# Optimization experiments

Hardware: AMD Instinct MI355X
Metric: run time of the kernel (lower is better)

Reference implementation:

```python
import jax, jax.numpy as jnp
import numpy as np
from jax import lax

BN_EPS = 1e-5


def _spatial_gate(x, w, g, b, m, v):
    # x: [N, C, H, W]; ChannelPool -> [N, 2, H, W]; 7x7 conv -> [N,1,H,W]; BN (eval); sigmoid gate
    comp = jnp.stack([jnp.max(x, axis=1), jnp.mean(x, axis=1)], axis=1)
    o = lax.conv_general_dilated(comp, w, (1, 1), [(3, 3), (3, 3)],
                                 dimension_numbers=('NCHW', 'OIHW', 'NCHW'))
    o = (o - m[None, :, None, None]) * lax.rsqrt(v + BN_EPS)[None, :, None, None] \
        * g[None, :, None, None] + b[None, :, None, None]
    s = jax.nn.sigmoid(o)
    return x * s


def _eca_sort(x, w_eca):
    # global avg pool -> sort channels desc -> 1D conv over sorted seq -> sigmoid -> unsort -> gate
    y = jnp.mean(x, axis=(2, 3))               # [N, C]
    order = jnp.argsort(-y, axis=1)            # descending sort indices
    rank = jnp.argsort(order, axis=1)          # inverse permutation
    ys = jnp.take_along_axis(y, order, axis=1)  # sorted descending
    k = w_eca.shape[-1]
    p = k // 2
    o = lax.conv_general_dilated(ys[:, None, :], w_eca, (1,), [(p, p)],
                                 dimension_numbers=('NCH', 'OIH', 'NCH'))[:, 0, :]
    sig = jax.nn.sigmoid(o)
    yr = jnp.take_along_axis(sig, rank, axis=1)  # reorder back per original index_select(rank)
    return x * yr[:, :, None, None]


def setup_inputs() -> dict:
    key = jax.random.key(0)
    ks = jax.random.split(key, 6)
    N, C, H, W = 32, 256, 56, 56
    inp = {
        'x': jax.random.normal(ks[0], (N, C, H, W), dtype=jnp.float32),
        'weight': jax.random.normal(ks[1], (1,), dtype=jnp.float32),
        'w_h': jax.random.normal(ks[2], (1, 2, 7, 7), dtype=jnp.float32) * 0.1,
        'g_h': jnp.ones((1,), jnp.float32), 'b_h': jnp.zeros((1,), jnp.float32),
        'm_h': jnp.zeros((1,), jnp.float32), 'v_h': jnp.ones((1,), jnp.float32),
        'w_w': jax.random.normal(ks[3], (1, 2, 7, 7), dtype=jnp.float32) * 0.1,
        'g_w': jnp.ones((1,), jnp.float32), 'b_w': jnp.zeros((1,), jnp.float32),
        'm_w': jnp.zeros((1,), jnp.float32), 'v_w': jnp.ones((1,), jnp.float32),
        'w_s': jax.random.normal(ks[4], (1, 2, 7, 7), dtype=jnp.float32) * 0.1,
        'g_s': jnp.ones((1,), jnp.float32), 'b_s': jnp.zeros((1,), jnp.float32),
        'm_s': jnp.zeros((1,), jnp.float32), 'v_s': jnp.ones((1,), jnp.float32),
        'w_eca': jax.random.normal(ks[5], (1, 1, 5), dtype=jnp.float32) * 0.3,
    }
    return inp


def reference(x, weight, w_h, g_h, b_h, m_h, v_h, w_w, g_w, b_w, m_w, v_w,
              w_s, g_s, b_s, m_s, v_s, w_eca):
    # branch 1: gate over H-as-channel (permute 0,2,1,3)
    xh = jnp.transpose(x, (0, 2, 1, 3))
    x11 = jnp.transpose(_spatial_gate(xh, w_h, g_h, b_h, m_h, v_h), (0, 2, 1, 3))
    # branch 2: gate over W-as-channel (permute 0,3,2,1)
    xw = jnp.transpose(x, (0, 3, 2, 1))
    x21 = jnp.transpose(_spatial_gate(xw, w_w, g_w, b_w, m_w, v_w), (0, 3, 2, 1))
    # branch 3: eca with sort/unsort
    x31 = _eca_sort(x, w_eca)
    # branch 4: plain spatial gate
    xo = _spatial_gate(x, w_s, g_s, b_s, m_s, v_s)
    return 0.23779 * xo + 0.24695 * x11 + 0.24365 * x21 + 0.27173 * x31
```

## Files before the change

### kernel.cpp

```cpp
#include <hip/hip_runtime.h>
#include <math.h>

#define N_ 32
#define C_ 256
#define H_ 56
#define W_ 56
#define HW_ (H_*W_)
#define HW4_ (HW_/4)
#define CHW_ (C_*HW_)
#define NHW_ (N_*HW_)
#define NHW4_ (NHW_/4)
#define NCW_ (N_*C_*W_)
#define NHC_ (N_*H_*C_)
#define BN_EPS_ 1e-5f

#define TLD 60
#define PLANES_PER_BLK 8
#define NB_PL 1024

#define SM_BUF1 3360
#define SM_CPMX 6720
#define SM_CPSM (6720 + 224)
#define SM_TOT  (6720 + 448)

#define F4MAX(a,b) do { (a).x=fmaxf((a).x,(b).x); (a).y=fmaxf((a).y,(b).y); \
                        (a).z=fmaxf((a).z,(b).z); (a).w=fmaxf((a).w,(b).w); } while(0)
#define F4ADD(a,b) do { (a).x+=(b).x; (a).y+=(b).y; (a).z+=(b).z; (a).w+=(b).w; } while(0)

__global__ __launch_bounds__(256) void pools_k(
        const float* __restrict__ x,
        float* __restrict__ maxH, float* __restrict__ meanH,
        float* __restrict__ maxW, float* __restrict__ meanW,
        float* __restrict__ pmx, float* __restrict__ psm,
        float* __restrict__ y) {
    __shared__ float smem[SM_TOT];
    int b = blockIdx.x;
    int tid = threadIdx.x;
    const float4* x4 = (const float4*)x;
    float* buf0 = smem;
    float* buf1 = smem + SM_BUF1;
    float* cpmx = smem + SM_CPMX;
    float* cpsm = smem + SM_CPSM;
    int pb0 = b * PLANES_PER_BLK;
    float4 r0, r1, r2, r3;
    int row0 = tid / 14,          col0 = (tid % 14) * 4;
    int row1 = (tid + 256) / 14,  col1 = ((tid + 256) % 14) * 4;
    int row2 = (tid + 512) / 14,  col2 = ((tid + 512) % 14) * 4;
    int row3 = (tid + 768) / 14,  col3 = ((tid + 768) % 14) * 4;
    float4 amx0, amx1, amx2, amx3, asm0, asm1, asm2, asm3;
    amx0 = amx1 = amx2 = amx3 = make_float4(-INFINITY, -INFINITY, -INFINITY, -INFINITY);
    asm0 = asm1 = asm2 = asm3 = make_float4(0.f, 0.f, 0.f, 0.f);
    {
        size_t base = (size_t)pb0 * HW4_;
        r0 = x4[base + tid];
        r1 = x4[base + 256 + tid];
        r2 = x4[base + 512 + tid];
        if (tid < 16) r3 = x4[base + 768 + tid];
        F4MAX(amx0, r0); F4ADD(asm0, r0);
        F4MAX(amx1, r1); F4ADD(asm1, r1);
        F4MAX(amx2, r2); F4ADD(asm2, r2);
        if (tid < 16) { F4MAX(amx3, r3); F4ADD(asm3, r3); }
        *(float4*)&buf0[row0 * TLD + col0] = r0;
        *(float4*)&buf0[row1 * TLD + col1] = r1;
        *(float4*)&buf0[row2 * TLD + col2] = r2;
        if (tid < 16) *(float4*)&buf0[row3 * TLD + col3] = r3;
    }
    __syncthreads();
    for (int k = 0; k < PLANES_PER_BLK; ++k) {
        float* cur = (k & 1) ? buf1 : buf0;
        float* nxt = (k & 1) ? buf0 : buf1;
        int pb = pb0 + k;
        int n = pb >> 8, c = pb & 255;
        if (k < PLANES_PER_BLK - 1) {
            size_t base = (size_t)(pb + 1) * HW4_;
            r0 = x4[base + tid];
            r1 = x4[base + 256 + tid];
            r2 = x4[base + 512 + tid];
            if (tid < 16) r3 = x4[base + 768 + tid];
        }
        if (tid < 224) {
            int w = tid % 56, hq = tid / 56;
            const float* base = &cur[(hq * 14) * TLD + w];
            float mx = -INFINITY, sm = 0.f;
            #pragma unroll
            for (int hh = 0; hh < 14; ++hh) {
                float v = base[hh * TLD];
                mx = fmaxf(mx, v); sm += v;
            }
            cpmx[hq * 56 + w] = mx;
            cpsm[hq * 56 + w] = sm;
        }
        __syncthreads();
        float colsum = 0.f;
        if (tid < 56) {
            float mx = cpmx[tid], sm = cpsm[tid];
            #pragma unroll
            for (int j = 1; j < 4; ++j) {
                mx = fmaxf(mx, cpmx[j * 56 + tid]);
                sm += cpsm[j * 56 + tid];
            }
            int o = (n * C_ + c) * W_ + tid;
            maxH[o] = mx;
            meanH[o] = sm * (1.f / H_);
            colsum = sm;
        }
        if (tid < 64) {
            float t = colsum;
            #pragma unroll
            for (int off = 32; off >= 1; off >>= 1) t += __shfl_xor(t, off);
            if (tid == 0) y[n * C_ + c] = t * (1.f / HW_);
        }
        if (tid < 224) {
            int h = tid >> 2, kq = tid & 3;
            const float* base = &cur[h * TLD + kq * 14];
            float mx = -INFINITY, sm = 0.f;
            #pragma unroll
            for (int kk = 0; kk < 14; ++kk) {
                float v = base[kk];
                mx = fmaxf(mx, v); sm += v;
            }
            mx = fmaxf(mx, __shfl_xor(mx, 1)); sm += __shfl_xor(sm, 1);
            mx = fmaxf(mx, __shfl_xor(mx, 2)); sm += __shfl_xor(sm, 2);
            if (kq == 0) {
                int o = (n * H_ + h) * C_ + c;
                maxW[o] = mx;
                meanW[o] = sm * (1.f / W_);
            }
        }
        if (k < PLANES_PER_BLK - 1) {
            F4MAX(amx0, r0); F4ADD(asm0, r0);
            F4MAX(amx1, r1); F4ADD(asm1, r1);
            F4MAX(amx2, r2); F4ADD(asm2, r2);
            if (tid < 16) { F4MAX(amx3, r3); F4ADD(asm3, r3); }
            *(float4*)&nxt[row0 * TLD + col0] = r0;
            *(float4*)&nxt[row1 * TLD + col1] = r1;
            *(float4*)&nxt[row2 * TLD + col2] = r2;
            if (tid < 16) *(float4*)&nxt[row3 * TLD + col3] = r3;
        }
        __syncthreads();
    }
    {
        float4* PM = (float4*)pmx + (size_t)b * HW4_;
        float4* PS = (float4*)psm + (size_t)b * HW4_;
        PM[tid] = amx0;        PS[tid] = asm0;
        PM[tid + 256] = amx1;  PS[tid + 256] = asm1;
        PM[tid + 512] = amx2;  PS[tid + 512] = asm2;
        if (tid < 16) { PM[tid + 768] = amx3; PS[tid + 768] = asm3; }
    }
}

__global__ __launch_bounds__(256) void cpool_final_k(
        const float* __restrict__ pmx, const float* __restrict__ psm,
        float* __restrict__ maxC, float* __restrict__ meanC) {
    int t = blockIdx.x * 256 + threadIdx.x;
    int n = t / HW4_, hw4 = t - n * HW4_;
    const float4* PM = (const float4*)pmx + (size_t)(n * 32) * HW4_ + hw4;
    const float4* PS = (const float4*)psm + (size_t)(n * 32) * HW4_ + hw4;
    float4 mx = make_float4(-INFINITY, -INFINITY, -INFINITY, -INFINITY);
    float4 sm = make_float4(0.f, 0.f, 0.f, 0.f);
    #pragma unroll 8
    for (int g = 0; g < 32; ++g) {
        float4 v = PM[(size_t)g * HW4_];
        float4 s = PS[(size_t)g * HW4_];
        F4MAX(mx, v);
        F4ADD(sm, s);
    }
    sm.x *= (1.f / C_); sm.y *= (1.f / C_); sm.z *= (1.f / C_); sm.w *= (1.f / C_);
    ((float4*)maxC)[t] = mx;
    ((float4*)meanC)[t] = sm;
}

template <int R, int Cc>
__device__ __forceinline__ void conv7_part(int t, const float* __restrict__ p0,
                                           const float* __restrict__ p1,
                                           const float* __restrict__ wt,
                                           float g, float bb, float m, float v,
                                           float* __restrict__ out) {
    const int per = R * Cc;
    int n = t / per;
    int r2 = t - n * per;
    int i = r2 / Cc, j = r2 - i * Cc;
    const float* b0 = p0 + (size_t)n * per;
    const float* b1 = p1 + (size_t)n * per;
    float acc = 0.f;
    #pragma unroll
    for (int ki = 0; ki < 7; ++ki) {
        int ii = i + ki - 3;
        if (ii < 0 || ii >= R) continue;
        #pragma unroll
        for (int kj = 0; kj < 7; ++kj) {
            int jj = j + kj - 3;
            if (jj < 0 || jj >= Cc) continue;
            int idx = ii * Cc + jj;
            acc += b0[idx] * wt[ki * 7 + kj] + b1[idx] * wt[49 + ki * 7 + kj];
        }
    }
    float o = (acc - m) * rsqrtf(v + BN_EPS_) * g + bb;
    out[t] = 1.f / (1.f + expf(-o));
}

#define NB_SS (NHW_ / 256)
#define NB_SH (NCW_ / 256)
#define NB_SW (NHC_ / 256)

__global__ __launch_bounds__(256) void conv_eca_k(
        const float* __restrict__ maxC, const float* __restrict__ meanC,
        const float* __restrict__ maxH, const float* __restrict__ meanH,
        const float* __restrict__ maxW, const float* __restrict__ meanW,
        const float* __restrict__ w_s, const float* __restrict__ g_s,
        const float* __restrict__ b_s, const float* __restrict__ m_s,
        const float* __restrict__ v_s,
        const float* __restrict__ w_h, const float* __restrict__ g_h,
        const float* __restrict__ b_h, const float* __restrict__ m_h,
        const float* __restrict__ v_h,
        const float* __restrict__ w_w, const float* __restrict__ g_w,
        const float* __restrict__ b_w, const float* __restrict__ m_w,
        const float* __restrict__ v_w,
        const float* __restrict__ y, const float* __restrict__ w_eca,
        float* __restrict__ s_s, float* __restrict__ s_h, float* __restrict__ s_w,
        float* __restrict__ gate) {
    __shared__ float sv[C_];
    __shared__ int si[C_];
    int b = blockIdx.x;
    int tid = threadIdx.x;
    if (b < NB_SS) {
        conv7_part<H_, W_>(b * 256 + tid, maxC, meanC, w_s, g_s[0], b_s[0], m_s[0],
                           v_s[0], s_s);
    } else if (b < NB_SS + NB_SH) {
        conv7_part<C_, W_>((b - NB_SS) * 256 + tid, maxH, meanH, w_h, g_h[0], b_h[0],
                           m_h[0], v_h[0], s_h);
    } else if (b < NB_SS + NB_SH + NB_SW) {
        conv7_part<H_, C_>((b - NB_SS - NB_SH) * 256 + tid, maxW, meanW, w_w, g_w[0],
                           b_w[0], m_w[0], v_w[0], s_w);
    } else {
        int n = b - (NB_SS + NB_SH + NB_SW);
        sv[tid] = y[n * C_ + tid];
        si[tid] = tid;
        __syncthreads();
        for (int k = 2; k <= C_; k <<= 1) {
            for (int j = k >> 1; j > 0; j >>= 1) {
                int ixj = tid ^ j;
                if (ixj > tid) {
                    float v1 = sv[tid], v2 = sv[ixj];
                    int i1 = si[tid], i2 = si[ixj];
                    bool before = (v1 > v2) || (v1 == v2 && i1 < i2);
                    bool dir = ((tid & k) == 0);
                    if (dir ? !before : before) {
                        sv[tid] = v2; sv[ixj] = v1;
                        si[tid] = i2; si[ixj] = i1;
                    }
                }
                __syncthreads();
            }
        }
        float o = 0.f;
        #pragma unroll
        for (int j = 0; j < 5; ++j) {
            int p = tid + j - 2;
            if (p >= 0 && p < C_) o += sv[p] * w_eca[j];
        }
        gate[n * C_ + si[tid]] = 1.f / (1.f + expf(-o));
    }
}

__global__ __launch_bounds__(256) void apply_k(
        const float* __restrict__ x, const float* __restrict__ s_s,
        const float* __restrict__ s_h, const float* __restrict__ s_w,
        const float* __restrict__ gate, float* __restrict__ out) {
    int t0 = blockIdx.x * 512 + threadIdx.x;
    #pragma unroll
    for (int r = 0; r < 2; ++r) {
        int t = t0 + r * 256;
        int f = t * 4;
        int n = f / CHW_;
        int rem = f - n * CHW_;
        int c = rem / HW_;
        int hw = rem - c * HW_;
        int h = hw / W_;
        int w = hw - h * W_;
        float4 xv = ((const float4*)x)[t];
        float4 s4 = *(const float4*)(s_s + (size_t)n * HW_ + hw);
        float4 h4 = *(const float4*)(s_h + ((size_t)n * C_ + c) * W_ + w);
        float sw = s_w[((size_t)n * H_ + h) * C_ + c];
        float ge = gate[n * C_ + c];
        float base = 0.24365f * sw + 0.27173f * ge;
        float4 o;
        o.x = xv.x * (0.23779f * s4.x + 0.24695f * h4.x + base);
        o.y = xv.y * (0.23779f * s4.y + 0.24695f * h4.y + base);
        o.z = xv.z * (0.23779f * s4.z + 0.24695f * h4.z + base);
        o.w = xv.w * (0.23779f * s4.w + 0.24695f * h4.w + base);
        ((float4*)out)[t] = o;
    }
}

extern "C" void kernel_launch(void* const* d_in, const int* in_sizes, int n_in,
                              void* d_out, int out_size, void* d_ws, size_t ws_size,
                              hipStream_t stream) {
    const float* x     = (const float*)d_in[0];
    const float* w_h   = (const float*)d_in[2];
    const float* g_h   = (const float*)d_in[3];
    const float* b_h   = (const float*)d_in[4];
    const float* m_h   = (const float*)d_in[5];
    const float* v_h   = (const float*)d_in[6];
    const float* w_w   = (const float*)d_in[7];
    const float* g_w   = (const float*)d_in[8];
    const float* b_w   = (const float*)d_in[9];
    const float* m_w   = (const float*)d_in[10];
    const float* v_w   = (const float*)d_in[11];
    const float* w_s   = (const float*)d_in[12];
    const float* g_s   = (const float*)d_in[13];
    const float* b_s   = (const float*)d_in[14];
    const float* m_s   = (const float*)d_in[15];
    const float* v_s   = (const float*)d_in[16];
    const float* w_eca = (const float*)d_in[17];
    float* out = (float*)d_out;

    float* ws    = (float*)d_ws;
    float* maxC  = ws;
    float* meanC = maxC  + NHW_;
    float* maxH  = meanC + NHW_;
    float* meanH = maxH  + NCW_;
    float* maxW  = meanH + NCW_;
    float* meanW = maxW  + NHC_;
    float* s_s   = meanW + NHC_;
    float* s_h   = s_s   + NHW_;
    float* s_w   = s_h   + NCW_;
    float* yv    = s_w   + NHC_;
    float* gate  = yv    + N_ * C_;
    float* pmx   = gate  + N_ * C_;
    float* psm   = pmx   + NB_PL * HW_;

    pools_k<<<NB_PL, 256, 0, stream>>>(x, maxH, meanH, maxW, meanW, pmx, psm, yv);

    cpool_final_k<<<NHW4_ / 256, 256, 0, stream>>>(pmx, psm, maxC, meanC);

    int conv_blocks = NB_SS + NB_SH + NB_SW + N_;
    conv_eca_k<<<conv_blocks, 256, 0, stream>>>(maxC, meanC, maxH, meanH, maxW, meanW,
                                                w_s, g_s, b_s, m_s, v_s,
                                                w_h, g_h, b_h, m_h, v_h,
                                                w_w, g_w, b_w, m_w, v_w,
                                                yv, w_eca, s_s, s_h, s_w, gate);

    apply_k<<<(N_ * CHW_ / 4) / 512, 256, 0, stream>>>(x, s_s, s_h, s_w, gate, out);
}
```

Measured before the change: 104.8 us.

## Store W-branch pooled maps channel-major and transpose conv weights accordingly

The W-branch pooled max/mean and its gate are now stored as [N,C,H] instead of [N,H,C]. The conv uses transposed weight indexing so the result is unchanged. The aim is coalesced stores in pools_k, where consecutive h map to contiguous addresses, and more local gate reads in apply_k. The W-pool computation is also moved before the barrier, and launch bounds with a minimum of 4 blocks are added to the two pooling kernels, which may constrain register allocation.

```diff
diff --git a/kernel.cpp b/kernel.cpp
--- a/kernel.cpp
+++ b/kernel.cpp
@@ -27,10 +27,10 @@
                         (a).z=fmaxf((a).z,(b).z); (a).w=fmaxf((a).w,(b).w); } while(0)
 #define F4ADD(a,b) do { (a).x+=(b).x; (a).y+=(b).y; (a).z+=(b).z; (a).w+=(b).w; } while(0)
 
-__global__ __launch_bounds__(256) void pools_k(
+__global__ __launch_bounds__(256, 4) void pools_k(
         const float* __restrict__ x,
         float* __restrict__ maxH, float* __restrict__ meanH,
-        float* __restrict__ maxW, float* __restrict__ meanW,
+        float* __restrict__ maxWt, float* __restrict__ meanWt,
         float* __restrict__ pmx, float* __restrict__ psm,
         float* __restrict__ y) {
     __shared__ float smem[SM_TOT];
@@ -90,6 +90,23 @@
             cpmx[hq * 56 + w] = mx;
             cpsm[hq * 56 + w] = sm;
         }
+        if (tid < 224) {
+            int h = tid >> 2, kq = tid & 3;
+            const float* base = &cur[h * TLD + kq * 14];
+            float mx = -INFINITY, sm = 0.f;
+            #pragma unroll
+            for (int kk = 0; kk < 14; ++kk) {
+                float v = base[kk];
+                mx = fmaxf(mx, v); sm += v;
+            }
+            mx = fmaxf(mx, __shfl_xor(mx, 1)); sm += __shfl_xor(sm, 1);
+            mx = fmaxf(mx, __shfl_xor(mx, 2)); sm += __shfl_xor(sm, 2);
+            if (kq == 0) {
+                int o = (n * C_ + c) * H_ + h;
+                maxWt[o] = mx;
+                meanWt[o] = sm * (1.f / W_);
+            }
+        }
         __syncthreads();
         float colsum = 0.f;
         if (tid < 56) {
@@ -109,23 +126,6 @@
             #pragma unroll
             for (int off = 32; off >= 1; off >>= 1) t += __shfl_xor(t, off);
             if (tid == 0) y[n * C_ + c] = t * (1.f / HW_);
-        }
-        if (tid < 224) {
-            int h = tid >> 2, kq = tid & 3;
-            const float* base = &cur[h * TLD + kq * 14];
-            float mx = -INFINITY, sm = 0.f;
-            #pragma unroll
-            for (int kk = 0; kk < 14; ++kk) {
-                float v = base[kk];
-                mx = fmaxf(mx, v); sm += v;
-            }
-            mx = fmaxf(mx, __shfl_xor(mx, 1)); sm += __shfl_xor(sm, 1);
-            mx = fmaxf(mx, __shfl_xor(mx, 2)); sm += __shfl_xor(sm, 2);
-            if (kq == 0) {
-                int o = (n * H_ + h) * C_ + c;
-                maxW[o] = mx;
-                meanW[o] = sm * (1.f / W_);
-            }
         }
         if (k < PLANES_PER_BLK - 1) {
             F4MAX(amx0, r0); F4ADD(asm0, r0);
@@ -149,7 +149,7 @@
     }
 }
 
-__global__ __launch_bounds__(256) void cpool_final_k(
+__global__ __launch_bounds__(256, 4) void cpool_final_k(
         const float* __restrict__ pmx, const float* __restrict__ psm,
         float* __restrict__ maxC, float* __restrict__ meanC) {
     int t = blockIdx.x * 256 + threadIdx.x;
@@ -170,7 +170,7 @@
     ((float4*)meanC)[t] = sm;
 }
 
-template <int R, int Cc>
+template <int R, int Cc, bool TR>
 __device__ __forceinline__ void conv7_part(int t, const float* __restrict__ p0,
                                            const float* __restrict__ p1,
                                            const float* __restrict__ wt,
@@ -192,7 +192,8 @@
             int jj = j + kj - 3;
             if (jj < 0 || jj >= Cc) continue;
             int idx = ii * Cc + jj;
-            acc += b0[idx] * wt[ki * 7 + kj] + b1[idx] * wt[49 + ki * 7 + kj];
+            int wi = TR ? (kj * 7 + ki) : (ki * 7 + kj);
+            acc += b0[idx] * wt[wi] + b1[idx] * wt[49 + wi];
         }
     }
     float o = (acc - m) * rsqrtf(v + BN_EPS_) * g + bb;
@@ -206,7 +207,7 @@
 __global__ __launch_bounds__(256) void conv_eca_k(
         const float* __restrict__ maxC, const float* __restrict__ meanC,
         const float* __restrict__ maxH, const float* __restrict__ meanH,
-        const float* __restrict__ maxW, const float* __restrict__ meanW,
+        const float* __restrict__ maxWt, const float* __restrict__ meanWt,
         const float* __restrict__ w_s, const float* __restrict__ g_s,
         const float* __restrict__ b_s, const float* __restrict__ m_s,
         const float* __restrict__ v_s,
@@ -217,21 +218,21 @@
         const float* __restrict__ b_w, const float* __restrict__ m_w,
         const float* __restrict__ v_w,
         const float* __restrict__ y, const float* __restrict__ w_eca,
-        float* __restrict__ s_s, float* __restrict__ s_h, float* __restrict__ s_w,
+        float* __restrict__ s_s, float* __restrict__ s_h, float* __restrict__ s_wt,
         float* __restrict__ gate) {
     __shared__ float sv[C_];
     __shared__ int si[C_];
     int b = blockIdx.x;
     int tid = threadIdx.x;
     if (b < NB_SS) {
-        conv7_part<H_, W_>(b * 256 + tid, maxC, meanC, w_s, g_s[0], b_s[0], m_s[0],
-                           v_s[0], s_s);
+        conv7_part<H_, W_, false>(b * 256 + tid, maxC, meanC, w_s, g_s[0], b_s[0],
+                                  m_s[0], v_s[0], s_s);
     } else if (b < NB_SS + NB_SH) {
-        conv7_part<C_, W_>((b - NB_SS) * 256 + tid, maxH, meanH, w_h, g_h[0], b_h[0],
-                           m_h[0], v_h[0], s_h);
+        conv7_part<C_, W_, false>((b - NB_SS) * 256 + tid, maxH, meanH, w_h, g_h[0],
+                                  b_h[0], m_h[0], v_h[0], s_h);
     } else if (b < NB_SS + NB_SH + NB_SW) {
-        conv7_part<H_, C_>((b - NB_SS - NB_SH) * 256 + tid, maxW, meanW, w_w, g_w[0],
-                           b_w[0], m_w[0], v_w[0], s_w);
+        conv7_part<C_, H_, true>((b - NB_SS - NB_SH) * 256 + tid, maxWt, meanWt, w_w,
+                                 g_w[0], b_w[0], m_w[0], v_w[0], s_wt);
     } else {
         int n = b - (NB_SS + NB_SH + NB_SW);
         sv[tid] = y[n * C_ + tid];
@@ -265,7 +266,7 @@
 
 __global__ __launch_bounds__(256) void apply_k(
         const float* __restrict__ x, const float* __restrict__ s_s,
-        const float* __restrict__ s_h, const float* __restrict__ s_w,
+        const float* __restrict__ s_h, const float* __restrict__ s_wt,
         const float* __restrict__ gate, float* __restrict__ out) {
     int t0 = blockIdx.x * 512 + threadIdx.x;
     #pragma unroll
@@ -281,7 +282,7 @@
         float4 xv = ((const float4*)x)[t];
         float4 s4 = *(const float4*)(s_s + (size_t)n * HW_ + hw);
         float4 h4 = *(const float4*)(s_h + ((size_t)n * C_ + c) * W_ + w);
-        float sw = s_w[((size_t)n * H_ + h) * C_ + c];
+        float sw = s_wt[((size_t)n * C_ + c) * H_ + h];
         float ge = gate[n * C_ + c];
         float base = 0.24365f * sw + 0.27173f * ge;
         float4 o;
@@ -320,26 +321,26 @@
     float* meanC = maxC  + NHW_;
     float* maxH  = meanC + NHW_;
     float* meanH = maxH  + NCW_;
-    float* maxW  = meanH + NCW_;
-    float* meanW = maxW  + NHC_;
-    float* s_s   = meanW + NHC_;
+    float* maxWt = meanH + NCW_;
+    float* meanWt= maxWt + NHC_;
+    float* s_s   = meanWt+ NHC_;
     float* s_h   = s_s   + NHW_;
-    float* s_w   = s_h   + NCW_;
-    float* yv    = s_w   + NHC_;
+    float* s_wt  = s_h   + NCW_;
+    float* yv    = s_wt  + NHC_;
     float* gate  = yv    + N_ * C_;
     float* pmx   = gate  + N_ * C_;
-    float* psm   = pmx   + NB_PL * HW_;
-
-    pools_k<<<NB_PL, 256, 0, stream>>>(x, maxH, meanH, maxW, meanW, pmx, psm, yv);
+    float* psm   = pmx   + (size_t)NB_PL * HW_;
+
+    pools_k<<<NB_PL, 256, 0, stream>>>(x, maxH, meanH, maxWt, meanWt, pmx, psm, yv);
 
     cpool_final_k<<<NHW4_ / 256, 256, 0, stream>>>(pmx, psm, maxC, meanC);
 
     int conv_blocks = NB_SS + NB_SH + NB_SW + N_;
-    conv_eca_k<<<conv_blocks, 256, 0, stream>>>(maxC, meanC, maxH, meanH, maxW, meanW,
+    conv_eca_k<<<conv_blocks, 256, 0, stream>>>(maxC, meanC, maxH, meanH, maxWt, meanWt,
                                                 w_s, g_s, b_s, m_s, v_s,
                                                 w_h, g_h, b_h, m_h, v_h,
                                                 w_w, g_w, b_w, m_w, v_w,
-                                                yv, w_eca, s_s, s_h, s_w, gate);
-
-    apply_k<<<(N_ * CHW_ / 4) / 512, 256, 0, stream>>>(x, s_s, s_h, s_w, gate, out);
-}
+                                                yv, w_eca, s_s, s_h, s_wt, gate);
+
+    apply_k<<<(N_ * CHW_ / 4) / 512, 256, 0, stream>>>(x, s_s, s_h, s_wt, gate, out);
+}
```

New measurement: 94.28 us. 10.1% less time.
